# Kernel optimization log

Measured on AMD Instinct MI355X. Metric: run time of the kernel, lower is better.

## Reference

```python
import jax, jax.numpy as jnp
import numpy as np

LB = 8      # luma bins
CM = 1      # channel multiplier
GC = 16     # guide complexity
NIN, NOUT = 4, 3
BN_EPS = 1e-5


def bilateral_slice(grid, guide):
    # grid: [B, gh, gw, gd, C]; guide: [B, H, W] in [0,1]
    B, gh, gw, gd, C = grid.shape
    _, H, W = guide.shape
    dt = guide.dtype
    hg = (jnp.arange(H, dtype=dt) + 0.5) * (gh / H) - 0.5   # [H]
    wg = (jnp.arange(W, dtype=dt) + 0.5) * (gw / W) - 0.5   # [W]
    zg = guide * gd - 0.5                                    # [B,H,W]
    h0 = jnp.floor(hg); w0 = jnp.floor(wg); z0 = jnp.floor(zg)
    fh = hg - h0; fw = wg - w0; fz = zg - z0
    h0 = h0.astype(jnp.int32); w0 = w0.astype(jnp.int32); z0 = z0.astype(jnp.int32)
    bidx = jnp.arange(B)[:, None, None]
    out = jnp.zeros((B, H, W, C), dtype=grid.dtype)
    for dh in (0, 1):
        hi = jnp.clip(h0 + dh, 0, gh - 1)          # [H]
        wh_h = fh if dh else (1.0 - fh)
        for dw in (0, 1):
            wi = jnp.clip(w0 + dw, 0, gw - 1)      # [W]
            wh_w = fw if dw else (1.0 - fw)
            w_hw = (wh_h[:, None] * wh_w[None, :])[None]  # [1,H,W]
            for dz in (0, 1):
                zi = jnp.clip(z0 + dz, 0, gd - 1)  # [B,H,W]
                wh_z = fz if dz else (1.0 - fz)
                g = grid[bidx, hi[None, :, None], wi[None, None, :], zi]  # [B,H,W,C]
                out = out + g * (w_hw * wh_z)[..., None]
    return out


def conv1x1(x, w, b):
    # x: [B,Cin,H,W], w: [Cout,Cin], b: [Cout]
    return jnp.einsum('oc,bchw->bohw', w, x) + b[None, :, None, None]


def setup_inputs() -> dict:
    key = jax.random.key(0)
    ks = jax.random.split(key, 12)
    B, H, W, GH, GW = 4, 1024, 1024, 16, 16
    fullres = jax.random.uniform(ks[0], (B, 3, H, W), dtype=jnp.float32)
    local_features = jax.random.normal(ks[1], (B, 8 * CM * LB, GH, GW), dtype=jnp.float32)
    global_features = jax.random.normal(ks[2], (B, 8 * CM * LB), dtype=jnp.float32)
    cout = LB * NOUT * NIN  # 96
    fusion_w = jax.random.normal(ks[3], (cout, 8 * CM * LB), dtype=jnp.float32) * 0.1
    fusion_b = jnp.zeros((cout,), dtype=jnp.float32)
    g1_w = jax.random.normal(ks[4], (GC, 3), dtype=jnp.float32) * 0.5
    g1_b = jnp.zeros((GC,), dtype=jnp.float32)
    bn_gamma = jnp.ones((GC,), dtype=jnp.float32)
    bn_beta = jnp.zeros((GC,), dtype=jnp.float32)
    bn_mean = jnp.zeros((GC,), dtype=jnp.float32)
    bn_var = jnp.ones((GC,), dtype=jnp.float32)
    g2_w = jax.random.normal(ks[5], (1, GC), dtype=jnp.float32) * 0.3
    g2_b = jnp.zeros((1,), dtype=jnp.float32)
    return dict(fullres=fullres, local_features=local_features, global_features=global_features,
                fusion_w=fusion_w, fusion_b=fusion_b, g1_w=g1_w, g1_b=g1_b,
                bn_gamma=bn_gamma, bn_beta=bn_beta, bn_mean=bn_mean, bn_var=bn_var,
                g2_w=g2_w, g2_b=g2_b)


def reference(fullres, local_features, global_features, fusion_w, fusion_b,
              g1_w, g1_b, bn_gamma, bn_beta, bn_mean, bn_var, g2_w, g2_b):
    B = fullres.shape[0]
    # Fusion: relu(local + broadcast global), then 1x1 conv to 96 channels
    fused = jax.nn.relu(local_features + global_features[:, :, None, None])
    x = conv1x1(fused, fusion_w, fusion_b)                    # [B,96,GH,GW]
    GH, GW = x.shape[2], x.shape[3]
    # split(12, dim=1) + stack(dim=2) -> [B,12,LB,GH,GW]
    coeffs = x.reshape(B, LB, NIN * NOUT, GH, GW).transpose(0, 2, 1, 3, 4)
    # GuideNN: 1x1 conv + BN(eval) + relu, then 1x1 conv + sigmoid
    g = conv1x1(fullres, g1_w, g1_b)
    g = (g - bn_mean[None, :, None, None]) * (bn_gamma[None, :, None, None] *
        jax.lax.rsqrt(bn_var + BN_EPS)[None, :, None, None]) + bn_beta[None, :, None, None]
    g = jax.nn.relu(g)
    guide = jax.nn.sigmoid(conv1x1(g, g2_w, g2_b))[:, 0]      # [B,H,W]
    # Slicing: permute grid to [B,GH,GW,LB,12], trilinear slice, back to NCHW
    grid = coeffs.transpose(0, 3, 4, 2, 1)
    sliced = bilateral_slice(grid, guide)                     # [B,H,W,12]
    coeff = sliced.transpose(0, 3, 1, 2)                      # [B,12,H,W]
    # ApplyCoeffs
    R = jnp.sum(fullres * coeff[:, 0:3], axis=1, keepdims=True) + coeff[:, 9:10]
    G = jnp.sum(fullres * coeff[:, 3:6], axis=1, keepdims=True) + coeff[:, 10:11]
    Bc = jnp.sum(fullres * coeff[:, 6:9], axis=1, keepdims=True) + coeff[:, 11:12]
    return jnp.tanh(jnp.concatenate([R, G, Bc], axis=1))
```

## Files before the change

kernel.cpp:

```cpp
#include <hip/hip_runtime.h>
#include <math.h>


#define GRIDBUF_FLOATS (4 * 16 * 16 * 96)
#define CELL_STRIDE 100

typedef float  vfloat4 __attribute__((ext_vector_type(4)));
typedef float  f2      __attribute__((ext_vector_type(2)));
typedef int    i2      __attribute__((ext_vector_type(2)));

__device__ inline f2 splat2(float x) { f2 v; v.x = x; v.y = x; return v; }

__device__ inline f2 fast_tanh2(f2 x) {
    f2 ax = __builtin_elementwise_abs(x);
    f2 xx = ax + ax;
    f2 e;
    e.x = __expf(xx.x);
    e.y = __expf(xx.y);
    f2 ep1 = e + splat2(1.0f);
    f2 r;
    r.x = __builtin_amdgcn_rcpf(ep1.x);
    r.y = __builtin_amdgcn_rcpf(ep1.y);
    f2 t = splat2(1.0f) - (r + r);
    i2 sgn = __builtin_bit_cast(i2, x) & (i2){(int)0x80000000, (int)0x80000000};
    return __builtin_bit_cast(f2, __builtin_bit_cast(i2, t) | sgn);
}

__global__ __launch_bounds__(128) void coeff_kernel(
    const float* __restrict__ lf,
    const float* __restrict__ gf,
    const float* __restrict__ fw,
    const float* __restrict__ fb,
    const float* __restrict__ g1w,
    const float* __restrict__ g1b,
    const float* __restrict__ bng,
    const float* __restrict__ bnb,
    const float* __restrict__ bnm,
    const float* __restrict__ bnv,
    const float* __restrict__ g2w,
    const float* __restrict__ g2b,
    float* __restrict__ gridbuf,
    float* __restrict__ params)
{
    __shared__ float fused[64];
    const int blk = blockIdx.x;
    const int b   = blk >> 8;
    const int pos = blk & 255;
    const int t   = threadIdx.x;

    if (t < 64) {
        float v = lf[(b * 64 + t) * 256 + pos] + gf[b * 64 + t];
        fused[t] = v > 0.0f ? v : 0.0f;
    }
    __syncthreads();

    if (t < 96) {
        float acc = fb[t];
        const float* wrow = fw + t * 64;
#pragma unroll
        for (int i = 0; i < 64; ++i) acc = fmaf(wrow[i], fused[i], acc);
        gridbuf[blk * 96 + t] = acc;
    }

    if (blk == 0 && t >= 96 && t < 112) {
        int k = t - 96;
        float a = bng[k] * rsqrtf(bnv[k] + 1e-5f);
        params[k]      = g1w[k * 3 + 0] * a;
        params[16 + k] = g1w[k * 3 + 1] * a;
        params[32 + k] = g1w[k * 3 + 2] * a;
        params[48 + k] = (g1b[k] - bnm[k]) * a + bnb[k];
        params[64 + k] = g2w[k];
        if (k == 0) params[80] = g2b[0];
    }
}

__global__ __launch_bounds__(256) void slice_apply_kernel(
    const float* __restrict__ fullres,
    const float* __restrict__ gridbuf,
    const float* __restrict__ params,
    float* __restrict__ out)
{
    __shared__ __align__(16) float hrow[16 * CELL_STRIDE];

    const int t = threadIdx.x;
    const int b = blockIdx.x >> 10;
    const int y = blockIdx.x & 1023;

    float hg = (y + 0.5f) * 0.015625f - 0.5f;
    int   h0 = (int)floorf(hg);
    float fh = hg - (float)h0;
    int hc0 = h0 < 0 ? 0 : h0;
    int hc1 = (h0 + 1) > 15 ? 15 : (h0 + 1);

    const float* row0 = gridbuf + (b * 256 + hc0 * 16) * 96;
    const float* row1 = gridbuf + (b * 256 + hc1 * 16) * 96;
    const float wfh0 = 1.0f - fh;
#pragma unroll
    for (int i4 = t; i4 < 384; i4 += 256) {
        const int i   = i4 << 2;
        const int wc  = i / 96;
        const int rem = i - wc * 96;
        float4 a = *(const float4*)(row0 + i);
        float4 c = *(const float4*)(row1 + i);
        float4 r;
        r.x = fmaf(wfh0, a.x, fh * c.x);
        r.y = fmaf(wfh0, a.y, fh * c.y);
        r.z = fmaf(wfh0, a.z, fh * c.z);
        r.w = fmaf(wfh0, a.w, fh * c.w);
        *(float4*)(hrow + wc * CELL_STRIDE + rem) = r;
    }
    __syncthreads();

    const int xb = t << 2;
    const int pixbase = (y << 10) + xb;
    const int planeB = (b * 3) << 20;

    const float4 r4 = *(const float4*)(fullres + planeB + (0 << 20) + pixbase);
    const float4 g4 = *(const float4*)(fullres + planeB + (1 << 20) + pixbase);
    const float4 b4 = *(const float4*)(fullres + planeB + (2 << 20) + pixbase);

    const int w0i = (xb < 32) ? -1 : ((xb - 32) >> 6);
    const int wc0 = w0i < 0 ? 0 : w0i;
    const int wc1 = (w0i + 1) > 15 ? 15 : (w0i + 1);
    const float* cell0 = hrow + wc0 * CELL_STRIDE;
    const float* cell1 = hrow + wc1 * CELL_STRIDE;

    float Rv[4], Gv[4], Bv[4];

#pragma unroll
    for (int pp = 0; pp < 2; ++pp) {
        f2 rr, gg, bb;
        if (pp == 0) { rr = (f2){r4.x, r4.y}; gg = (f2){g4.x, g4.y}; bb = (f2){b4.x, b4.y}; }
        else         { rr = (f2){r4.z, r4.w}; gg = (f2){g4.z, g4.w}; bb = (f2){b4.z, b4.w}; }

        f2 acc = splat2(params[80]);
#pragma unroll
        for (int k = 0; k < 16; ++k) {
            f2 gk = __builtin_elementwise_fma(rr, splat2(params[k]),
                    __builtin_elementwise_fma(gg, splat2(params[16 + k]),
                    __builtin_elementwise_fma(bb, splat2(params[32 + k]),
                                              splat2(params[48 + k]))));
            gk = __builtin_elementwise_max(gk, splat2(0.0f));
            acc = __builtin_elementwise_fma(gk, splat2(params[64 + k]), acc);
        }
        f2 zg;
        zg.x = fmaf(8.0f, __builtin_amdgcn_rcpf(1.0f + __expf(-acc.x)), -0.5f);
        zg.y = fmaf(8.0f, __builtin_amdgcn_rcpf(1.0f + __expf(-acc.y)), -0.5f);

#pragma unroll
        for (int px = 0; px < 2; ++px) {
            const int j = pp * 2 + px;
            const float zgp = px ? zg.y : zg.x;
            int   z0 = (int)floorf(zgp);
            float fz = zgp - (float)z0;
            int zc0 = z0 < 0 ? 0 : z0;
            int zc1 = (z0 + 1) > 7 ? 7 : (z0 + 1);

            const int x = xb + j;
            const float fw_ = (float)x * 0.015625f + (0.0078125f - 0.5f) - (float)w0i;
            const float ww0 = 1.0f - fw_;
            const f2 W00 = splat2(ww0 * (1.0f - fz));
            const f2 W01 = splat2(ww0 * fz);
            const f2 W10 = splat2(fw_ * (1.0f - fz));
            const f2 W11 = splat2(fw_ * fz);

            const float4* p00 = (const float4*)(cell0 + zc0 * 12);
            const float4* p01 = (const float4*)(cell0 + zc1 * 12);
            const float4* p10 = (const float4*)(cell1 + zc0 * 12);
            const float4* p11 = (const float4*)(cell1 + zc1 * 12);

            f2 sa[6];
#pragma unroll
            for (int q = 0; q < 3; ++q) {
                float4 a = p00[q], c = p01[q], d = p10[q], e = p11[q];
                f2 alo = (f2){a.x, a.y}, ahi = (f2){a.z, a.w};
                f2 clo = (f2){c.x, c.y}, chi = (f2){c.z, c.w};
                f2 dlo = (f2){d.x, d.y}, dhi = (f2){d.z, d.w};
                f2 elo = (f2){e.x, e.y}, ehi = (f2){e.z, e.w};
                sa[2 * q] =
                    __builtin_elementwise_fma(alo, W00,
                    __builtin_elementwise_fma(clo, W01,
                    __builtin_elementwise_fma(dlo, W10, elo * W11)));
                sa[2 * q + 1] =
                    __builtin_elementwise_fma(ahi, W00,
                    __builtin_elementwise_fma(chi, W01,
                    __builtin_elementwise_fma(dhi, W10, ehi * W11)));
            }

            const float r  = px ? rr.y : rr.x;
            const float g  = px ? gg.y : gg.x;
            const float bl = px ? bb.y : bb.x;
            Rv[j] = fmaf(r, sa[0].x, fmaf(g, sa[0].y, fmaf(bl, sa[1].x, sa[4].y)));
            Gv[j] = fmaf(r, sa[1].y, fmaf(g, sa[2].x, fmaf(bl, sa[2].y, sa[5].x)));
            Bv[j] = fmaf(r, sa[3].x, fmaf(g, sa[3].y, fmaf(bl, sa[4].x, sa[5].y)));
        }
    }

    f2 tR0 = fast_tanh2((f2){Rv[0], Rv[1]});
    f2 tR1 = fast_tanh2((f2){Rv[2], Rv[3]});
    f2 tG0 = fast_tanh2((f2){Gv[0], Gv[1]});
    f2 tG1 = fast_tanh2((f2){Gv[2], Gv[3]});
    f2 tB0 = fast_tanh2((f2){Bv[0], Bv[1]});
    f2 tB1 = fast_tanh2((f2){Bv[2], Bv[3]});

    vfloat4 vR = {tR0.x, tR0.y, tR1.x, tR1.y};
    vfloat4 vG = {tG0.x, tG0.y, tG1.x, tG1.y};
    vfloat4 vB = {tB0.x, tB0.y, tB1.x, tB1.y};
    __builtin_nontemporal_store(vR, (vfloat4*)(out + planeB + (0 << 20) + pixbase));
    __builtin_nontemporal_store(vG, (vfloat4*)(out + planeB + (1 << 20) + pixbase));
    __builtin_nontemporal_store(vB, (vfloat4*)(out + planeB + (2 << 20) + pixbase));
}

extern "C" void kernel_launch(void* const* d_in, const int* in_sizes, int n_in,
                              void* d_out, int out_size, void* d_ws, size_t ws_size,
                              hipStream_t stream) {
    const float* fullres = (const float*)d_in[0];
    const float* lf      = (const float*)d_in[1];
    const float* gf      = (const float*)d_in[2];
    const float* fw      = (const float*)d_in[3];
    const float* fb      = (const float*)d_in[4];
    const float* g1w     = (const float*)d_in[5];
    const float* g1b     = (const float*)d_in[6];
    const float* bng     = (const float*)d_in[7];
    const float* bnb     = (const float*)d_in[8];
    const float* bnm     = (const float*)d_in[9];
    const float* bnv     = (const float*)d_in[10];
    const float* g2w     = (const float*)d_in[11];
    const float* g2b     = (const float*)d_in[12];
    float* out = (float*)d_out;

    float* gridbuf = (float*)d_ws;
    float* params  = gridbuf + GRIDBUF_FLOATS;

    coeff_kernel<<<4 * 256, 128, 0, stream>>>(lf, gf, fw, fb, g1w, g1b,
                                              bng, bnb, bnm, bnv, g2w, g2b,
                                              gridbuf, params);
    slice_apply_kernel<<<4 * 1024, 256, 0, stream>>>(fullres, gridbuf, params, out);
}
```

Baseline: 133.6 us.

## Process four rows per block with per-row h-interpolated grid slices in LDS

```diff
diff --git a/kernel.cpp b/kernel.cpp
--- a/kernel.cpp
+++ b/kernel.cpp
@@ -4,6 +4,7 @@
 
 #define GRIDBUF_FLOATS (4 * 16 * 16 * 96)
 #define CELL_STRIDE 100
+#define ROW_STRIDE  1600
 
 typedef float  vfloat4 __attribute__((ext_vector_type(4)));
 typedef float  f2      __attribute__((ext_vector_type(2)));
@@ -80,135 +81,144 @@
     const float* __restrict__ params,
     float* __restrict__ out)
 {
-    __shared__ __align__(16) float hrow[16 * CELL_STRIDE];
-
-    const int t = threadIdx.x;
-    const int b = blockIdx.x >> 10;
-    const int y = blockIdx.x & 1023;
-
-    float hg = (y + 0.5f) * 0.015625f - 0.5f;
-    int   h0 = (int)floorf(hg);
-    float fh = hg - (float)h0;
-    int hc0 = h0 < 0 ? 0 : h0;
-    int hc1 = (h0 + 1) > 15 ? 15 : (h0 + 1);
-
-    const float* row0 = gridbuf + (b * 256 + hc0 * 16) * 96;
-    const float* row1 = gridbuf + (b * 256 + hc1 * 16) * 96;
-    const float wfh0 = 1.0f - fh;
-#pragma unroll
-    for (int i4 = t; i4 < 384; i4 += 256) {
-        const int i   = i4 << 2;
-        const int wc  = i / 96;
-        const int rem = i - wc * 96;
-        float4 a = *(const float4*)(row0 + i);
-        float4 c = *(const float4*)(row1 + i);
-        float4 r;
-        r.x = fmaf(wfh0, a.x, fh * c.x);
-        r.y = fmaf(wfh0, a.y, fh * c.y);
-        r.z = fmaf(wfh0, a.z, fh * c.z);
-        r.w = fmaf(wfh0, a.w, fh * c.w);
-        *(float4*)(hrow + wc * CELL_STRIDE + rem) = r;
+    __shared__ __align__(16) float hrow[4 * ROW_STRIDE];
+
+    const int t     = threadIdx.x;
+    const int b     = blockIdx.x >> 8;
+    const int ytile = (blockIdx.x & 255) << 2;
+
+    {
+        const int r    = t >> 6;
+        const int lane = t & 63;
+        const int y    = ytile + r;
+        const int h0i  = (y < 32) ? -1 : ((y - 32) >> 6);
+        const float fh = ((float)y * 0.015625f + (0.0078125f - 0.5f)) - (float)h0i;
+        const int hc0  = h0i < 0 ? 0 : h0i;
+        const int hc1  = (h0i + 1) > 15 ? 15 : (h0i + 1);
+        const float* row0 = gridbuf + (b * 256 + hc0 * 16) * 96;
+        const float* row1 = gridbuf + (b * 256 + hc1 * 16) * 96;
+        const float wfh0 = 1.0f - fh;
+        float* dst = hrow + r * ROW_STRIDE;
+#pragma unroll
+        for (int k = 0; k < 6; ++k) {
+            const int i4  = lane + (k << 6);
+            const int i   = i4 << 2;
+            const int wc  = i / 96;
+            const int rem = i - wc * 96;
+            float4 a = *(const float4*)(row0 + i);
+            float4 c = *(const float4*)(row1 + i);
+            float4 rr;
+            rr.x = fmaf(wfh0, a.x, fh * c.x);
+            rr.y = fmaf(wfh0, a.y, fh * c.y);
+            rr.z = fmaf(wfh0, a.z, fh * c.z);
+            rr.w = fmaf(wfh0, a.w, fh * c.w);
+            *(float4*)(dst + wc * CELL_STRIDE + rem) = rr;
+        }
     }
     __syncthreads();
 
     const int xb = t << 2;
-    const int pixbase = (y << 10) + xb;
-    const int planeB = (b * 3) << 20;
-
-    const float4 r4 = *(const float4*)(fullres + planeB + (0 << 20) + pixbase);
-    const float4 g4 = *(const float4*)(fullres + planeB + (1 << 20) + pixbase);
-    const float4 b4 = *(const float4*)(fullres + planeB + (2 << 20) + pixbase);
-
     const int w0i = (xb < 32) ? -1 : ((xb - 32) >> 6);
     const int wc0 = w0i < 0 ? 0 : w0i;
     const int wc1 = (w0i + 1) > 15 ? 15 : (w0i + 1);
-    const float* cell0 = hrow + wc0 * CELL_STRIDE;
-    const float* cell1 = hrow + wc1 * CELL_STRIDE;
-
-    float Rv[4], Gv[4], Bv[4];
-
-#pragma unroll
-    for (int pp = 0; pp < 2; ++pp) {
-        f2 rr, gg, bb;
-        if (pp == 0) { rr = (f2){r4.x, r4.y}; gg = (f2){g4.x, g4.y}; bb = (f2){b4.x, b4.y}; }
-        else         { rr = (f2){r4.z, r4.w}; gg = (f2){g4.z, g4.w}; bb = (f2){b4.z, b4.w}; }
-
-        f2 acc = splat2(params[80]);
-#pragma unroll
-        for (int k = 0; k < 16; ++k) {
-            f2 gk = __builtin_elementwise_fma(rr, splat2(params[k]),
-                    __builtin_elementwise_fma(gg, splat2(params[16 + k]),
-                    __builtin_elementwise_fma(bb, splat2(params[32 + k]),
-                                              splat2(params[48 + k]))));
-            gk = __builtin_elementwise_max(gk, splat2(0.0f));
-            acc = __builtin_elementwise_fma(gk, splat2(params[64 + k]), acc);
+    const float fw0 = (float)xb * 0.015625f + (0.0078125f - 0.5f) - (float)w0i;
+
+    const int planeB = (b * 3) << 20;
+
+    for (int r = 0; r < 4; ++r) {
+        const int y = ytile + r;
+        const int pixbase = (y << 10) + xb;
+        const float* cell0 = hrow + r * ROW_STRIDE + wc0 * CELL_STRIDE;
+        const float* cell1 = hrow + r * ROW_STRIDE + wc1 * CELL_STRIDE;
+
+        const float4 r4 = *(const float4*)(fullres + planeB + (0 << 20) + pixbase);
+        const float4 g4 = *(const float4*)(fullres + planeB + (1 << 20) + pixbase);
+        const float4 b4 = *(const float4*)(fullres + planeB + (2 << 20) + pixbase);
+
+        float Rv[4], Gv[4], Bv[4];
+
+#pragma unroll
+        for (int pp = 0; pp < 2; ++pp) {
+            f2 rr, gg, bb;
+            if (pp == 0) { rr = (f2){r4.x, r4.y}; gg = (f2){g4.x, g4.y}; bb = (f2){b4.x, b4.y}; }
+            else         { rr = (f2){r4.z, r4.w}; gg = (f2){g4.z, g4.w}; bb = (f2){b4.z, b4.w}; }
+
+            f2 acc = splat2(params[80]);
+#pragma unroll
+            for (int k = 0; k < 16; ++k) {
+                f2 gk = __builtin_elementwise_fma(rr, splat2(params[k]),
+                        __builtin_elementwise_fma(gg, splat2(params[16 + k]),
+                        __builtin_elementwise_fma(bb, splat2(params[32 + k]),
+                                                  splat2(params[48 + k]))));
+                gk = __builtin_elementwise_max(gk, splat2(0.0f));
+                acc = __builtin_elementwise_fma(gk, splat2(params[64 + k]), acc);
+            }
+            f2 zg;
+            zg.x = fmaf(8.0f, __builtin_amdgcn_rcpf(1.0f + __expf(-acc.x)), -0.5f);
+            zg.y = fmaf(8.0f, __builtin_amdgcn_rcpf(1.0f + __expf(-acc.y)), -0.5f);
+
+#pragma unroll
+            for (int px = 0; px < 2; ++px) {
+                const int j = pp * 2 + px;
+                const float zgp = px ? zg.y : zg.x;
+                int   z0 = (int)floorf(zgp);
+                float fz = zgp - (float)z0;
+                int zc0 = z0 < 0 ? 0 : z0;
+                int zc1 = (z0 + 1) > 7 ? 7 : (z0 + 1);
+
+                const float fw_ = fw0 + (float)j * 0.015625f;
+                const float ww0 = 1.0f - fw_;
+                const f2 W00 = splat2(ww0 * (1.0f - fz));
+                const f2 W01 = splat2(ww0 * fz);
+                const f2 W10 = splat2(fw_ * (1.0f - fz));
+                const f2 W11 = splat2(fw_ * fz);
+
+                const float4* p00 = (const float4*)(cell0 + zc0 * 12);
+                const float4* p01 = (const float4*)(cell0 + zc1 * 12);
+                const float4* p10 = (const float4*)(cell1 + zc0 * 12);
+                const float4* p11 = (const float4*)(cell1 + zc1 * 12);
+
+                f2 sa[6];
+#pragma unroll
+                for (int q = 0; q < 3; ++q) {
+                    float4 a = p00[q], c = p01[q], d = p10[q], e = p11[q];
+                    f2 alo = (f2){a.x, a.y}, ahi = (f2){a.z, a.w};
+                    f2 clo = (f2){c.x, c.y}, chi = (f2){c.z, c.w};
+                    f2 dlo = (f2){d.x, d.y}, dhi = (f2){d.z, d.w};
+                    f2 elo = (f2){e.x, e.y}, ehi = (f2){e.z, e.w};
+                    sa[2 * q] =
+                        __builtin_elementwise_fma(alo, W00,
+                        __builtin_elementwise_fma(clo, W01,
+                        __builtin_elementwise_fma(dlo, W10, elo * W11)));
+                    sa[2 * q + 1] =
+                        __builtin_elementwise_fma(ahi, W00,
+                        __builtin_elementwise_fma(chi, W01,
+                        __builtin_elementwise_fma(dhi, W10, ehi * W11)));
+                }
+
+                const float rs  = px ? rr.y : rr.x;
+                const float gs  = px ? gg.y : gg.x;
+                const float bs  = px ? bb.y : bb.x;
+                Rv[j] = fmaf(rs, sa[0].x, fmaf(gs, sa[0].y, fmaf(bs, sa[1].x, sa[4].y)));
+                Gv[j] = fmaf(rs, sa[1].y, fmaf(gs, sa[2].x, fmaf(bs, sa[2].y, sa[5].x)));
+                Bv[j] = fmaf(rs, sa[3].x, fmaf(gs, sa[3].y, fmaf(bs, sa[4].x, sa[5].y)));
+            }
         }
-        f2 zg;
-        zg.x = fmaf(8.0f, __builtin_amdgcn_rcpf(1.0f + __expf(-acc.x)), -0.5f);
-        zg.y = fmaf(8.0f, __builtin_amdgcn_rcpf(1.0f + __expf(-acc.y)), -0.5f);
-
-#pragma unroll
-        for (int px = 0; px < 2; ++px) {
-            const int j = pp * 2 + px;
-            const float zgp = px ? zg.y : zg.x;
-            int   z0 = (int)floorf(zgp);
-            float fz = zgp - (float)z0;
-            int zc0 = z0 < 0 ? 0 : z0;
-            int zc1 = (z0 + 1) > 7 ? 7 : (z0 + 1);
-
-            const int x = xb + j;
-            const float fw_ = (float)x * 0.015625f + (0.0078125f - 0.5f) - (float)w0i;
-            const float ww0 = 1.0f - fw_;
-            const f2 W00 = splat2(ww0 * (1.0f - fz));
-            const f2 W01 = splat2(ww0 * fz);
-            const f2 W10 = splat2(fw_ * (1.0f - fz));
-            const f2 W11 = splat2(fw_ * fz);
-
-            const float4* p00 = (const float4*)(cell0 + zc0 * 12);
-            const float4* p01 = (const float4*)(cell0 + zc1 * 12);
-            const float4* p10 = (const float4*)(cell1 + zc0 * 12);
-            const float4* p11 = (const float4*)(cell1 + zc1 * 12);
-
-            f2 sa[6];
-#pragma unroll
-            for (int q = 0; q < 3; ++q) {
-                float4 a = p00[q], c = p01[q], d = p10[q], e = p11[q];
-                f2 alo = (f2){a.x, a.y}, ahi = (f2){a.z, a.w};
-                f2 clo = (f2){c.x, c.y}, chi = (f2){c.z, c.w};
-                f2 dlo = (f2){d.x, d.y}, dhi = (f2){d.z, d.w};
-                f2 elo = (f2){e.x, e.y}, ehi = (f2){e.z, e.w};
-                sa[2 * q] =
-                    __builtin_elementwise_fma(alo, W00,
-                    __builtin_elementwise_fma(clo, W01,
-                    __builtin_elementwise_fma(dlo, W10, elo * W11)));
-                sa[2 * q + 1] =
-                    __builtin_elementwise_fma(ahi, W00,
-                    __builtin_elementwise_fma(chi, W01,
-                    __builtin_elementwise_fma(dhi, W10, ehi * W11)));
-            }
-
-            const float r  = px ? rr.y : rr.x;
-            const float g  = px ? gg.y : gg.x;
-            const float bl = px ? bb.y : bb.x;
-            Rv[j] = fmaf(r, sa[0].x, fmaf(g, sa[0].y, fmaf(bl, sa[1].x, sa[4].y)));
-            Gv[j] = fmaf(r, sa[1].y, fmaf(g, sa[2].x, fmaf(bl, sa[2].y, sa[5].x)));
-            Bv[j] = fmaf(r, sa[3].x, fmaf(g, sa[3].y, fmaf(bl, sa[4].x, sa[5].y)));
-        }
-    }
-
-    f2 tR0 = fast_tanh2((f2){Rv[0], Rv[1]});
-    f2 tR1 = fast_tanh2((f2){Rv[2], Rv[3]});
-    f2 tG0 = fast_tanh2((f2){Gv[0], Gv[1]});
-    f2 tG1 = fast_tanh2((f2){Gv[2], Gv[3]});
-    f2 tB0 = fast_tanh2((f2){Bv[0], Bv[1]});
-    f2 tB1 = fast_tanh2((f2){Bv[2], Bv[3]});
-
-    vfloat4 vR = {tR0.x, tR0.y, tR1.x, tR1.y};
-    vfloat4 vG = {tG0.x, tG0.y, tG1.x, tG1.y};
-    vfloat4 vB = {tB0.x, tB0.y, tB1.x, tB1.y};
-    __builtin_nontemporal_store(vR, (vfloat4*)(out + planeB + (0 << 20) + pixbase));
-    __builtin_nontemporal_store(vG, (vfloat4*)(out + planeB + (1 << 20) + pixbase));
-    __builtin_nontemporal_store(vB, (vfloat4*)(out + planeB + (2 << 20) + pixbase));
+
+        f2 tR0 = fast_tanh2((f2){Rv[0], Rv[1]});
+        f2 tR1 = fast_tanh2((f2){Rv[2], Rv[3]});
+        f2 tG0 = fast_tanh2((f2){Gv[0], Gv[1]});
+        f2 tG1 = fast_tanh2((f2){Gv[2], Gv[3]});
+        f2 tB0 = fast_tanh2((f2){Bv[0], Bv[1]});
+        f2 tB1 = fast_tanh2((f2){Bv[2], Bv[3]});
+
+        vfloat4 vR = {tR0.x, tR0.y, tR1.x, tR1.y};
+        vfloat4 vG = {tG0.x, tG0.y, tG1.x, tG1.y};
+        vfloat4 vB = {tB0.x, tB0.y, tB1.x, tB1.y};
+        __builtin_nontemporal_store(vR, (vfloat4*)(out + planeB + (0 << 20) + pixbase));
+        __builtin_nontemporal_store(vG, (vfloat4*)(out + planeB + (1 << 20) + pixbase));
+        __builtin_nontemporal_store(vB, (vfloat4*)(out + planeB + (2 << 20) + pixbase));
+    }
 }
 
 extern "C" void kernel_launch(void* const* d_in, const int* in_sizes, int n_in,
@@ -235,5 +245,5 @@
     coeff_kernel<<<4 * 256, 128, 0, stream>>>(lf, gf, fw, fb, g1w, g1b,
                                               bng, bnb, bnm, bnv, g2w, g2b,
                                               gridbuf, params);
-    slice_apply_kernel<<<4 * 1024, 256, 0, stream>>>(fullres, gridbuf, params, out);
-}
+    slice_apply_kernel<<<4 * 256, 256, 0, stream>>>(fullres, gridbuf, params, out);
+}
```

Result: slower. 140.6 us (+5.2%).
